# Optimization experiments

Measured on AMD Instinct MI355X. Metric: run time of the kernel, lower is better.

## Reference

```python
import jax, jax.numpy as jnp
import numpy as np

N_DYADIC = 0   # init kwarg n: dyadic refinement order (0 = no refinement)


def _sig_kernel_gram(X, Y):
    """Signature-kernel Gram matrix via Goursat PDE solve (solver=0, linear kernel).

    X: (A, M, D), Y: (B, N, D). Returns K: (A, B) with K[a,b] = k_sig(x^a, y^b).
    PDE scheme: K[i+1,j+1] = K[i+1,j] + K[i,j+1] + K[i,j]*(inc[i,j] - 1),
    K[0,:] = K[:,0] = 1, inc[i,j] = <x_{i+1}-x_i, y_{j+1}-y_j>.
    The j-recursion is a prefix sum, so each row update is a vectorized cumsum;
    only the i-direction is sequential (lax.scan over M-1 rows).
    """
    dtype = X.dtype
    dX = X[:, 1:, :] - X[:, :-1, :]          # (A, M-1, D)
    dY = Y[:, 1:, :] - Y[:, :-1, :]          # (B, N-1, D)
    inc = jnp.einsum('amd,bnd->abmn', dX, dY)  # (A, B, M-1, N-1) increment grid
    if N_DYADIC > 0:
        f = 2 ** N_DYADIC
        inc = jnp.repeat(jnp.repeat(inc, f, axis=2), f, axis=3) / (f * f)
    A, B, M1, N1 = inc.shape
    ones_col = jnp.ones((A, B, 1), dtype)
    k0 = jnp.ones((A, B, N1 + 1), dtype)      # boundary row K[0, :] = 1

    def step(k_prev, inc_row):
        # k_new[j+1] = k_new[j] + (k_prev[j+1] - k_prev[j] + k_prev[j]*inc[j])
        delta = k_prev[..., 1:] - k_prev[..., :-1] + k_prev[..., :-1] * inc_row
        k_new = jnp.concatenate([ones_col, 1.0 + jnp.cumsum(delta, axis=-1)], axis=-1)
        return k_new, None

    k_last, _ = jax.lax.scan(step, k0, jnp.moveaxis(inc, 2, 0))
    return k_last[..., -1]                    # (A, B): K(s=T, t=T)


def setup_inputs() -> dict:
    key = jax.random.key(0)
    kx, ky = jax.random.split(key)
    # scale 0.1 keeps path increments moderate so the PDE solution stays well-conditioned
    X = jax.random.normal(kx, (64, 128, 64), dtype=jnp.float32) * 0.1
    Y = jax.random.normal(ky, (64, 128, 64), dtype=jnp.float32) * 0.1
    return {"X": X, "Y": Y}


def reference(X, Y):
    K_XX = _sig_kernel_gram(X, X)
    K_YY = _sig_kernel_gram(Y, Y)
    K_XY = _sig_kernel_gram(X, Y)
    dist = jnp.mean(K_XX) + jnp.mean(K_YY) - 2.0 * jnp.mean(K_XY)
    return jnp.mean((X[:, 0, :] - Y[:, 0, :]) ** 2) + dist
```

## Files before the change

### kernel.cpp

```cpp
#include <hip/hip_runtime.h>

#define AA   64
#define MM   128
#define DD   64
#define M1   127
#define CSTR 132
#define NXY  1024
#define NTRI 544
#define NBLK (NXY + 2*NTRI)
#define REG_I4 65536
#define PART_OFF (4u << 20)

typedef float f32x4 __attribute__((ext_vector_type(4)));
typedef short bf8_t __attribute__((ext_vector_type(8)));

template <int CTRL, int RM>
__device__ __forceinline__ float dpp0(float x) {
    return __int_as_float(
        __builtin_amdgcn_update_dpp(0, __float_as_int(x), CTRL, RM, 0xF, false));
}

__device__ __forceinline__ unsigned bf16_rne(float v) {
    unsigned u = __float_as_uint(v);
    return (u + 0x7FFFu + ((u >> 16) & 1u)) >> 16;
}
__device__ __forceinline__ float bf16_tof(unsigned h) {
    return __uint_as_float(h << 16);
}

__global__ __launch_bounds__(256) void prep_frags(const float* __restrict__ X,
                                                  const float* __restrict__ Y,
                                                  int4* __restrict__ frag) {
    const int tid = threadIdx.x, lane = tid & 63, w = tid >> 6;
    const int W    = blockIdx.x * 4 + w;
    const int inp  = W >> 9;
    const int p    = (W >> 3) & 63;
    const int tile = W & 7;
    const float* S = (inp ? Y : X) + p * (MM * DD);
    int i = tile * 16 + (lane & 15);
    if (i > 126) i = 126;
    const int d0 = (lane >> 4) << 3;

    int4* hi = frag + (inp * 2 + 0) * REG_I4;
    int4* lo = frag + (inp * 2 + 1) * REG_I4;
    const int base = p * 1024 + tile * 128 + lane;

    #pragma unroll
    for (int ks = 0; ks < 2; ++ks) {
        const float* r0 = S + i * DD + ks * 32 + d0;
        const float* r1 = r0 + DD;
        float4 a0 = *(const float4*)r0;
        float4 a1 = *(const float4*)(r0 + 4);
        float4 c0 = *(const float4*)r1;
        float4 c1 = *(const float4*)(r1 + 4);
        float v[8] = {c0.x - a0.x, c0.y - a0.y, c0.z - a0.z, c0.w - a0.w,
                      c1.x - a1.x, c1.y - a1.y, c1.z - a1.z, c1.w - a1.w};
        unsigned hs[8], ls[8];
        #pragma unroll
        for (int e = 0; e < 8; ++e) {
            hs[e] = bf16_rne(v[e]);
            ls[e] = bf16_rne(v[e] - bf16_tof(hs[e]));
        }
        int4 h, l;
        h.x = hs[0] | (hs[1] << 16); h.y = hs[2] | (hs[3] << 16);
        h.z = hs[4] | (hs[5] << 16); h.w = hs[6] | (hs[7] << 16);
        l.x = ls[0] | (ls[1] << 16); l.y = ls[2] | (ls[3] << 16);
        l.z = ls[4] | (ls[5] << 16); l.w = ls[6] | (ls[7] << 16);
        hi[base + ks * 64] = h;
        lo[base + ks * 64] = l;
    }
}

__global__ __launch_bounds__(256, 2)
void sig_pde(const int4* __restrict__ frag, float* __restrict__ partials) {
    const int tid = threadIdx.x, lane = tid & 63, w = tid >> 6;
    const int gid = blockIdx.x;

    int a, b, ain, bin;
    float wgt;
    if (gid < NXY) {
        b = gid >> 4; a = ((gid & 15) << 2) | w;
        ain = 0; bin = 1;
        wgt = -2.0f / 4096.0f;
    } else {
        int t = gid - NXY;
        int inp = 0;
        if (t >= NTRI) { t -= NTRI; inp = 1; }
        int q = (int)((__builtin_sqrtf((float)(2 * t + 1)) - 1.0f) * 0.5f);
        while (2 * (q + 1) * (q + 2) <= t) ++q;
        while (q > 0 && 2 * q * (q + 1) > t) --q;
        int r  = t - 2 * q * (q + 1);
        int i  = r / (q + 1);
        int ag = r - i * (q + 1);
        b = 4 * q + i; a = 4 * ag + w;
        ain = bin = inp;
        wgt = (a < b) ? (2.0f / 4096.0f) : ((a == b) ? (1.0f / 4096.0f) : 0.0f);
    }

    __shared__ int4  Bh[1024], Bl[1024];
    __shared__ float incS[4][16 * CSTR];
    __shared__ float red4[4];

    {
        const int4* Bhg = frag + (bin * 2 + 0) * REG_I4 + b * 1024;
        const int4* Blg = frag + (bin * 2 + 1) * REG_I4 + b * 1024;
        #pragma unroll
        for (int c = 0; c < 4; ++c) {
            int idx = c * 256 + tid;
            Bh[idx] = Bhg[idx];
            Bl[idx] = Blg[idx];
        }
    }
    __syncthreads();

    const int4* Ahg = frag + (ain * 2 + 0) * REG_I4 + a * 1024;
    const int4* Alg = frag + (ain * 2 + 1) * REG_I4 + a * 1024;

    int4 Ah[2], Al[2], Ahn[2], Aln[2];
    Ah[0] = Ahg[lane];      Ah[1] = Ahg[64 + lane];
    Al[0] = Alg[lane];      Al[1] = Alg[64 + lane];

    float k0 = 1.0f, k1 = 1.0f;
    float* incW = &incS[w][0];
    const int c2l = lane << 1;
    const int r0w = (lane >> 4) << 2, c0w = lane & 15;

    for (int strip = 0; strip < 8; ++strip) {
        if (strip < 7) {
            int off = (strip + 1) * 128 + lane;
            Ahn[0] = Ahg[off]; Ahn[1] = Ahg[off + 64];
            Aln[0] = Alg[off]; Aln[1] = Alg[off + 64];
        }

        f32x4 acc[8];
        #pragma unroll
        for (int t = 0; t < 8; ++t) acc[t] = (f32x4){0.f, 0.f, 0.f, 0.f};
        #pragma unroll
        for (int s = 0; s < 2; ++s) {
            bf8_t ah = __builtin_bit_cast(bf8_t, Ah[s]);
            bf8_t al = __builtin_bit_cast(bf8_t, Al[s]);
            #pragma unroll
            for (int t = 0; t < 8; ++t) {
                int fb = (t * 2 + s) * 64 + lane;
                bf8_t bh = *(const bf8_t*)&Bh[fb];
                bf8_t bl = *(const bf8_t*)&Bl[fb];
                acc[t] = __builtin_amdgcn_mfma_f32_16x16x32_bf16(ah, bh, acc[t], 0, 0, 0);
                acc[t] = __builtin_amdgcn_mfma_f32_16x16x32_bf16(ah, bl, acc[t], 0, 0, 0);
                acc[t] = __builtin_amdgcn_mfma_f32_16x16x32_bf16(al, bh, acc[t], 0, 0, 0);
            }
        }

        #pragma unroll
        for (int t = 0; t < 8; ++t) {
            float* pb = incW + r0w * CSTR + (t << 4) + c0w;
            pb[0]        = acc[t][0];
            pb[CSTR]     = acc[t][1];
            pb[2 * CSTR] = acc[t][2];
            pb[3 * CSTR] = acc[t][3];
        }

        const int rmax = (strip == 7) ? 15 : 16;
        for (int r = 0; r < rmax; ++r) {
            float2 sv = *(const float2*)(incW + r * CSTR + c2l);
            float s0 = sv.x, s1 = sv.y;
            float kp2 = dpp0<0x130, 0xF>(k0);
            float e0  = k1 - k0 + k0 * s0;
            float e1  = (lane < 63) ? (kp2 - k1 + k1 * s1) : 0.0f;
            float S = e0 + e1;
            S += dpp0<0x111, 0xF>(S);
            S += dpp0<0x112, 0xF>(S);
            S += dpp0<0x114, 0xF>(S);
            S += dpp0<0x118, 0xF>(S);
            S += dpp0<0x142, 0xA>(S);
            S += dpp0<0x143, 0xC>(S);
            float Sp = dpp0<0x138, 0xF>(S);
            k0 = 1.0f + Sp;
            k1 = 1.0f + S - e1;
        }

        Ah[0] = Ahn[0]; Ah[1] = Ahn[1];
        Al[0] = Aln[0]; Al[1] = Aln[1];
    }

    if (lane == 63) red4[w] = wgt * k1;
    __syncthreads();
    if (tid == 0)
        partials[gid] = red4[0] + red4[1] + red4[2] + red4[3];
}

__global__ void final_sum(const float* __restrict__ X, const float* __restrict__ Y,
                          const float* __restrict__ partials, float* __restrict__ out) {
    __shared__ float red[4];
    int tid = threadIdx.x;
    float acc = 0.f;
    for (int e = tid; e < NBLK; e += 256) acc += partials[e];
    for (int e = tid; e < AA * DD; e += 256) {
        int aa = e >> 6, d = e & 63;
        float df = X[aa * (MM * DD) + d] - Y[aa * (MM * DD) + d];
        acc = fmaf(df * df, 1.0f / 4096.0f, acc);
    }
    #pragma unroll
    for (int off = 32; off > 0; off >>= 1) acc += __shfl_down(acc, off);
    if ((tid & 63) == 0) red[tid >> 6] = acc;
    __syncthreads();
    if (tid == 0) out[0] = red[0] + red[1] + red[2] + red[3];
}

extern "C" void kernel_launch(void* const* d_in, const int* in_sizes, int n_in,
                              void* d_out, int out_size, void* d_ws, size_t ws_size,
                              hipStream_t stream) {
    const float* X = (const float*)d_in[0];
    const float* Y = (const float*)d_in[1];
    float* out = (float*)d_out;
    int4*  frag = (int4*)d_ws;
    float* partials = (float*)((char*)d_ws + PART_OFF);

    hipLaunchKernelGGL(prep_frags, dim3(256), dim3(256), 0, stream, X, Y, frag);
    hipLaunchKernelGGL(sig_pde, dim3(NBLK), dim3(256), 0, stream, frag, partials);
    hipLaunchKernelGGL(final_sum, dim3(1), dim3(256), 0, stream, X, Y, partials, out);
}
```

Baseline: 162.4 us.

## Overlap next strip-pair MFMA with the row recurrence and shorten the dependent chain

Each pass now computes two 16-row increment strips at once with interleaved MFMAs, so independent accumulator chains can hide MFMA latency. The MFMA for the next pair is issued between the LDS load and the scan of the current second strip, so matrix work can overlap the serial DPP prefix-scan chain. The recurrence is also rewritten algebraically: carrying the prefix sum and the previous e terms removes the cross-lane k shift and turns each update into one fma per element. The cost is higher register pressure from two accumulator sets and 16 buffered float2 rows, which may reduce occupancy under launch_bounds(256,2).

```diff
diff --git a/kernel.cpp b/kernel.cpp
--- a/kernel.cpp
+++ b/kernel.cpp
@@ -68,6 +68,36 @@
         l.z = ls[4] | (ls[5] << 16); l.w = ls[6] | (ls[7] << 16);
         hi[base + ks * 64] = h;
         lo[base + ks * 64] = l;
+    }
+}
+
+template <int ROWS>
+__device__ __forceinline__ void load_sv(const float* incW, int c2l, float2* sv) {
+    #pragma unroll
+    for (int r = 0; r < ROWS; ++r)
+        sv[r] = *(const float2*)(incW + r * CSTR + c2l);
+}
+
+template <int ROWS>
+__device__ __forceinline__ void chain_sv(const float2* sv, int lane,
+                                         float& Sv, float& e0p, float& e1p) {
+    #pragma unroll
+    for (int r = 0; r < ROWS; ++r) {
+        float s0 = sv[r].x;
+        float s1 = (lane < 63) ? sv[r].y : 0.0f;
+        float Sp  = dpp0<0x138, 0xF>(Sv);
+        float k0v = 1.0f + Sp;
+        float k1v = 1.0f + Sv - e1p;
+        float e0  = fmaf(k0v, s0, e0p);
+        float e1  = fmaf(k1v, s1, e1p);
+        float S   = e0 + e1;
+        S += dpp0<0x111, 0xF>(S);
+        S += dpp0<0x112, 0xF>(S);
+        S += dpp0<0x114, 0xF>(S);
+        S += dpp0<0x118, 0xF>(S);
+        S += dpp0<0x142, 0xA>(S);
+        S += dpp0<0x143, 0xC>(S);
+        Sv = S; e0p = e0; e1p = e1;
     }
 }
 
@@ -116,76 +146,91 @@
     const int4* Ahg = frag + (ain * 2 + 0) * REG_I4 + a * 1024;
     const int4* Alg = frag + (ain * 2 + 1) * REG_I4 + a * 1024;
 
-    int4 Ah[2], Al[2], Ahn[2], Aln[2];
-    Ah[0] = Ahg[lane];      Ah[1] = Ahg[64 + lane];
-    Al[0] = Alg[lane];      Al[1] = Alg[64 + lane];
-
-    float k0 = 1.0f, k1 = 1.0f;
+    int4 Ah[2][2], Al[2][2];
+    f32x4 acc[2][8];
+    float Sv = 0.0f, e0p = 0.0f, e1p = 0.0f;
+
     float* incW = &incS[w][0];
     const int c2l = lane << 1;
     const int r0w = (lane >> 4) << 2, c0w = lane & 15;
 
-    for (int strip = 0; strip < 8; ++strip) {
-        if (strip < 7) {
-            int off = (strip + 1) * 128 + lane;
-            Ahn[0] = Ahg[off]; Ahn[1] = Ahg[off + 64];
-            Aln[0] = Alg[off]; Aln[1] = Alg[off + 64];
-        }
-
-        f32x4 acc[8];
-        #pragma unroll
-        for (int t = 0; t < 8; ++t) acc[t] = (f32x4){0.f, 0.f, 0.f, 0.f};
-        #pragma unroll
-        for (int s = 0; s < 2; ++s) {
-            bf8_t ah = __builtin_bit_cast(bf8_t, Ah[s]);
-            bf8_t al = __builtin_bit_cast(bf8_t, Al[s]);
-            #pragma unroll
-            for (int t = 0; t < 8; ++t) {
-                int fb = (t * 2 + s) * 64 + lane;
-                bf8_t bh = *(const bf8_t*)&Bh[fb];
-                bf8_t bl = *(const bf8_t*)&Bl[fb];
-                acc[t] = __builtin_amdgcn_mfma_f32_16x16x32_bf16(ah, bh, acc[t], 0, 0, 0);
-                acc[t] = __builtin_amdgcn_mfma_f32_16x16x32_bf16(ah, bl, acc[t], 0, 0, 0);
-                acc[t] = __builtin_amdgcn_mfma_f32_16x16x32_bf16(al, bh, acc[t], 0, 0, 0);
-            }
-        }
-
-        #pragma unroll
-        for (int t = 0; t < 8; ++t) {
-            float* pb = incW + r0w * CSTR + (t << 4) + c0w;
-            pb[0]        = acc[t][0];
-            pb[CSTR]     = acc[t][1];
-            pb[2 * CSTR] = acc[t][2];
-            pb[3 * CSTR] = acc[t][3];
-        }
-
-        const int rmax = (strip == 7) ? 15 : 16;
-        for (int r = 0; r < rmax; ++r) {
-            float2 sv = *(const float2*)(incW + r * CSTR + c2l);
-            float s0 = sv.x, s1 = sv.y;
-            float kp2 = dpp0<0x130, 0xF>(k0);
-            float e0  = k1 - k0 + k0 * s0;
-            float e1  = (lane < 63) ? (kp2 - k1 + k1 * s1) : 0.0f;
-            float S = e0 + e1;
-            S += dpp0<0x111, 0xF>(S);
-            S += dpp0<0x112, 0xF>(S);
-            S += dpp0<0x114, 0xF>(S);
-            S += dpp0<0x118, 0xF>(S);
-            S += dpp0<0x142, 0xA>(S);
-            S += dpp0<0x143, 0xC>(S);
-            float Sp = dpp0<0x138, 0xF>(S);
-            k0 = 1.0f + Sp;
-            k1 = 1.0f + S - e1;
-        }
-
-        Ah[0] = Ahn[0]; Ah[1] = Ahn[1];
-        Al[0] = Aln[0]; Al[1] = Aln[1];
-    }
-
-    if (lane == 63) red4[w] = wgt * k1;
+#define MFMA_PASS() do {                                                        \
+    _Pragma("unroll")                                                           \
+    for (int st_ = 0; st_ < 2; ++st_)                                           \
+        _Pragma("unroll")                                                       \
+        for (int t_ = 0; t_ < 8; ++t_) acc[st_][t_] = (f32x4){0.f,0.f,0.f,0.f}; \
+    _Pragma("unroll")                                                           \
+    for (int s_ = 0; s_ < 2; ++s_) {                                            \
+        bf8_t ah0 = __builtin_bit_cast(bf8_t, Ah[0][s_]);                       \
+        bf8_t al0 = __builtin_bit_cast(bf8_t, Al[0][s_]);                       \
+        bf8_t ah1 = __builtin_bit_cast(bf8_t, Ah[1][s_]);                       \
+        bf8_t al1 = __builtin_bit_cast(bf8_t, Al[1][s_]);                       \
+        _Pragma("unroll")                                                       \
+        for (int t_ = 0; t_ < 8; ++t_) {                                        \
+            int fb = (t_ * 2 + s_) * 64 + lane;                                 \
+            bf8_t bh = *(const bf8_t*)&Bh[fb];                                  \
+            bf8_t bl = *(const bf8_t*)&Bl[fb];                                  \
+            acc[0][t_] = __builtin_amdgcn_mfma_f32_16x16x32_bf16(ah0, bh, acc[0][t_], 0, 0, 0); \
+            acc[1][t_] = __builtin_amdgcn_mfma_f32_16x16x32_bf16(ah1, bh, acc[1][t_], 0, 0, 0); \
+            acc[0][t_] = __builtin_amdgcn_mfma_f32_16x16x32_bf16(ah0, bl, acc[0][t_], 0, 0, 0); \
+            acc[1][t_] = __builtin_amdgcn_mfma_f32_16x16x32_bf16(ah1, bl, acc[1][t_], 0, 0, 0); \
+            acc[0][t_] = __builtin_amdgcn_mfma_f32_16x16x32_bf16(al0, bh, acc[0][t_], 0, 0, 0); \
+            acc[1][t_] = __builtin_amdgcn_mfma_f32_16x16x32_bf16(al1, bh, acc[1][t_], 0, 0, 0); \
+        }                                                                       \
+    }                                                                           \
+} while (0)
+
+#define STORE_STRIP(st) do {                                   \
+    _Pragma("unroll")                                          \
+    for (int t_ = 0; t_ < 8; ++t_) {                           \
+        float* pb = incW + r0w * CSTR + (t_ << 4) + c0w;       \
+        pb[0]        = acc[st][t_][0];                         \
+        pb[CSTR]     = acc[st][t_][1];                         \
+        pb[2 * CSTR] = acc[st][t_][2];                         \
+        pb[3 * CSTR] = acc[st][t_][3];                         \
+    }                                                          \
+} while (0)
+
+#define LOAD_A(poff) do {                                      \
+    int off = (poff) + lane;                                   \
+    Ah[0][0] = Ahg[off];       Ah[0][1] = Ahg[off + 64];       \
+    Al[0][0] = Alg[off];       Al[0][1] = Alg[off + 64];       \
+    Ah[1][0] = Ahg[off + 128]; Ah[1][1] = Ahg[off + 192];      \
+    Al[1][0] = Alg[off + 128]; Al[1][1] = Alg[off + 192];      \
+} while (0)
+
+    LOAD_A(0);
+    MFMA_PASS();
+
+    for (int pass = 0; pass < 4; ++pass) {
+        STORE_STRIP(0);
+        if (pass < 3) LOAD_A((pass + 1) * 256);
+        {
+            float2 sv[16];
+            load_sv<16>(incW, c2l, sv);
+            chain_sv<16>(sv, lane, Sv, e0p, e1p);
+        }
+        STORE_STRIP(1);
+        if (pass < 3) {
+            float2 sv[16];
+            load_sv<16>(incW, c2l, sv);
+            MFMA_PASS();
+            chain_sv<16>(sv, lane, Sv, e0p, e1p);
+        } else {
+            float2 sv[15];
+            load_sv<15>(incW, c2l, sv);
+            chain_sv<15>(sv, lane, Sv, e0p, e1p);
+        }
+    }
+
+    if (lane == 63) red4[w] = wgt * (1.0f + Sv - e1p);
     __syncthreads();
     if (tid == 0)
         partials[gid] = red4[0] + red4[1] + red4[2] + red4[3];
+
+#undef MFMA_PASS
+#undef STORE_STRIP
+#undef LOAD_A
 }
 
 __global__ void final_sum(const float* __restrict__ X, const float* __restrict__ Y,
```

Result: faster. 147.6 us (-9.1%).
